# Optimization experiments

Hardware: AMD Instinct MI355X
Metric: run time of the kernel (lower is better)

## Reference

```python
import jax, jax.numpy as jnp
import numpy as np

NBINS = (128, 64, 32)
N_REGIONS = 5000
N_REGIONS_OI = 500
N_POINTS = 262144
SUM_H = sum(NBINS)            # 224
SUM_W = sum(n - 1 for n in NBINS)  # 221


def _spline_level(x, uw_region, uh_pt, local_ix):
    """One quadratic-spline level.
    x: [N] inputs in [0,1); uw_region: [R, n-1] region unnormalized widths;
    uh_pt: [N, n] per-point unnormalized heights (embedding + delta);
    local_ix: [N] int mapping points -> rows of uw_region.
    """
    # region-level widths / bin locations (calculate_widths / calculate_bin_locations)
    widths = jax.nn.softmax(uw_region, axis=-1)                # [R, n-1]
    bl = jnp.cumsum(widths, axis=-1)
    bl = bl.at[:, -1].set(1.0)
    bin_locations = jnp.pad(bl, ((0, 0), (1, 0)))              # [R, n]

    # gather per point (index_select(0, local_region_ix))
    widths_pt = widths[local_ix]                               # [N, n-1]
    bin_loc_pt = bin_locations[local_ix]                       # [N, n]

    # calculate_heights: exp then normalize so trapezoid integral == 1
    he = jnp.exp(uh_pt)                                        # [N, n]
    area = jnp.sum(0.5 * (he[:, :-1] + he[:, 1:]) * widths_pt, axis=-1, keepdims=True)
    heights = he / area                                        # [N, n]

    # calculate_bin_left_cdf
    cdf = jnp.cumsum(0.5 * (heights[:, :-1] + heights[:, 1:]) * widths_pt, axis=-1)
    cdf = cdf.at[:, -1].set(1.0)
    bin_left_cdf = jnp.pad(cdf, ((0, 0), (1, 0)))              # [N, n]

    # searchsorted(bin_locations, x, side='left') - 1, clamped to valid bins
    n = bin_loc_pt.shape[-1]
    bin_idx = jnp.clip(jnp.sum(bin_loc_pt < x[:, None], axis=-1) - 1, 0, n - 2)  # [N]

    take = lambda a, i: jnp.take_along_axis(a, i[:, None], axis=-1)[:, 0]
    in_loc = take(bin_loc_pt, bin_idx)
    in_w = take(widths_pt, bin_idx)
    in_cdf = take(bin_left_cdf, bin_idx)
    h_l = take(heights, bin_idx)
    h_r = take(heights, bin_idx + 1)

    alpha = (x - in_loc) / in_w
    a = 0.5 * (h_r - h_l) * in_w
    b = h_l * in_w
    out = a * alpha * alpha + b * alpha + in_cdf
    logabsdet = jnp.log(alpha * (h_r - h_l) + h_l)
    return out, logabsdet


def setup_inputs() -> dict:
    key = jax.random.key(0)
    k1, k2, k3, k4, k5, k6 = jax.random.split(key, 6)
    x = jax.random.uniform(k1, (N_POINTS,), dtype=jnp.float32)
    regions_oi = jax.random.randint(k2, (N_REGIONS_OI,), 0, N_REGIONS, dtype=jnp.int32)
    local_region_ix = jax.random.randint(k3, (N_POINTS,), 0, N_REGIONS_OI, dtype=jnp.int32)
    delta = jax.random.normal(k4, (N_POINTS, SUM_H), dtype=jnp.float32)
    # learned sparse embedding tables (init to random for a nontrivial baseline)
    heights_emb = 0.1 * jax.random.normal(k5, (N_REGIONS, SUM_H), dtype=jnp.float32)
    widths_emb = 0.1 * jax.random.normal(k6, (N_REGIONS, SUM_W), dtype=jnp.float32)
    return {"x": x, "regions_oi": regions_oi, "local_region_ix": local_region_ix,
            "delta": delta, "heights_emb": heights_emb, "widths_emb": widths_emb}


def reference(x, regions_oi, local_region_ix, delta, heights_emb, widths_emb):
    uh_all = heights_emb[regions_oi]   # [R, 224]
    uw_all = widths_emb[regions_oi]    # [R, 221]
    out = x
    logdet = jnp.zeros_like(x)
    oh = 0
    ow = 0
    for n in NBINS:
        uw = uw_all[:, ow:ow + (n - 1)]                               # [R, n-1]
        uh_pt = uh_all[local_region_ix][:, oh:oh + n] + delta[:, oh:oh + n]  # [N, n]
        out, ld = _spline_level(out, uw, uh_pt, local_region_ix)
        logdet = logdet + ld
        oh += n
        ow += n - 1
    return out, logdet
```

## Files before the change

### kernel.cpp

```cpp
#include <hip/hip_runtime.h>

#define NPOINTS 262144
#define SUMH 224
#define SUMW 221
#define NREG 500

__device__ __forceinline__ float rlane(float v, int l) {
  return __int_as_float(__builtin_amdgcn_readlane(__float_as_int(v), l));
}
template<int CTRL>
__device__ __forceinline__ float dpp0(float x) {
  return __int_as_float(__builtin_amdgcn_update_dpp(0, __float_as_int(x), CTRL, 0xF, 0xF, true));
}
template<int CTRL, int RM>
__device__ __forceinline__ float dpp_rm(float x) {
  return __int_as_float(__builtin_amdgcn_update_dpp(0, __float_as_int(x), CTRL, RM, 0xF, false));
}
template<int CTRL>
__device__ __forceinline__ float dpp_max_(float x) {
  return fmaxf(x, __int_as_float(__builtin_amdgcn_update_dpp(__float_as_int(x), __float_as_int(x), CTRL, 0xF, 0xF, false)));
}
__device__ __forceinline__ float wave_sum(float x) {
  x += dpp0<0x111>(x); x += dpp0<0x112>(x); x += dpp0<0x114>(x); x += dpp0<0x118>(x);
  x += dpp_rm<0x142, 0xA>(x); x += dpp_rm<0x143, 0xC>(x);
  return rlane(x, 63);
}
__device__ __forceinline__ float wave_max(float x) {
  x = dpp_max_<0x111>(x); x = dpp_max_<0x112>(x); x = dpp_max_<0x114>(x);
  x = dpp_max_<0x118>(x); x = dpp_max_<0x142>(x); x = dpp_max_<0x143>(x);
  return rlane(x, 63);
}
__device__ __forceinline__ float wave_scan_incl(float x) {
  x += dpp0<0x111>(x); x += dpp0<0x112>(x); x += dpp0<0x114>(x); x += dpp0<0x118>(x);
  x += dpp_rm<0x142, 0xA>(x);
  x += dpp_rm<0x143, 0xC>(x);
  return x;
}
__device__ __forceinline__ float grp32_sum(float x) {
  x += dpp0<0xB1>(x);
  x += dpp0<0x4E>(x);
  x += dpp0<0x141>(x);
  x += dpp0<0x140>(x);
  x += __int_as_float(__builtin_amdgcn_ds_swizzle(__float_as_int(x), 0x401F));
  return x;
}
__device__ __forceinline__ float bperm(int byteidx, float v) {
  return __int_as_float(__builtin_amdgcn_ds_bpermute(byteidx, __float_as_int(v)));
}

template<int M, int SRC, int DST, int NB>
__device__ __forceinline__ void region_level(const float* __restrict__ wrow,
    float* __restrict__ BL, float* __restrict__ HW, float* __restrict__ HS,
    int lane, float* lds)
{
  float v0 = (lane < M) ? wrow[SRC + lane] : -1e30f;
  float v1 = -1e30f;
  if constexpr (NB == 128) { if (lane + 64 < M) v1 = wrow[SRC + lane + 64]; }
  float m = wave_max(fmaxf(v0, v1));
  float e0 = __expf(v0 - m);
  float e1 = (NB == 128) ? __expf(v1 - m) : 0.0f;
  float sm = wave_sum(e0 + e1);
  float inv = 1.0f / sm;
  if (lane < NB) lds[lane] = e0;
  if constexpr (NB == 128) lds[lane + 64] = e1;
  __syncthreads();
  if (lane < NB) {
    HW[DST + lane] = 0.5f * e0 * inv;
    float prev = (lane == 0) ? 0.0f : lds[lane - 1];
    HS[DST + lane] = 0.5f * (e0 + prev) * inv;
  }
  if constexpr (NB == 128) {
    HW[DST + lane + 64] = 0.5f * e1 * inv;
    HS[DST + lane + 64] = 0.5f * (e1 + lds[lane + 63]) * inv;
  }
  float incl0 = wave_scan_incl(e0);
  if (lane == 0) BL[DST] = 0.0f;
  if (lane < M) BL[DST + 1 + lane] = (lane == M - 1) ? 1.0f : incl0 * inv;
  if constexpr (NB == 128) {
    float incl1 = wave_scan_incl(e1) + rlane(incl0, 63);
    int k = 64 + lane;
    if (k < M) BL[DST + 1 + k] = (k == M - 1) ? 1.0f : incl1 * inv;
  }
  __syncthreads();
}

__global__ void __launch_bounds__(64) region_kernel(
    const int* __restrict__ roi, const float* __restrict__ wemb,
    float* __restrict__ wsBL, float* __restrict__ wsHW, float* __restrict__ wsHS)
{
  __shared__ float lds[128];
  int rix = blockIdx.x;
  int lane = threadIdx.x;
  int greg = roi[rix];
  const float* wrow = wemb + (size_t)greg * SUMW;
  float* BL = wsBL + (size_t)rix * SUMH;
  float* HW = wsHW + (size_t)rix * SUMH;
  float* HS = wsHS + (size_t)rix * SUMH;
  region_level<127,   0,   0, 128>(wrow, BL, HW, HS, lane, lds);
  region_level< 63, 127, 128,  64>(wrow, BL, HW, HS, lane, lds);
  region_level< 31, 190, 192,  32>(wrow, BL, HW, HS, lane, lds);
}


struct PtState {
  float4 a0, b0, e0, f0, g0;
  float2 a1, b1, e1, f1, g1;
  float  a2, b2, e2, f2, g2;
  float  xv;
  int    pid;
};

__device__ __forceinline__ void load_pt(PtState& P, int pid, int s,
    const float* __restrict__ x, const int* __restrict__ lix,
    const int* __restrict__ roi, const float* __restrict__ delta,
    const float* __restrict__ hemb, const float* __restrict__ wsBL,
    const float* __restrict__ wsHW, const float* __restrict__ wsHS)
{
  P.pid = pid;
  P.xv = x[pid];
  int r = lix[pid];
  int greg = roi[r];
  const float* U  = hemb + (size_t)greg * SUMH;
  const float* D  = delta + (size_t)pid * SUMH;
  const float* BL = wsBL + (size_t)r * SUMH;
  const float* HW = wsHW + (size_t)r * SUMH;
  const float* HS = wsHS + (size_t)r * SUMH;
  int c0 = s * 4;
  P.a0 = *(const float4*)(U + c0);  P.b0 = *(const float4*)(D + c0);
  P.e0 = *(const float4*)(BL + c0); P.f0 = *(const float4*)(HW + c0);
  P.g0 = *(const float4*)(HS + c0);
  int c1 = 128 + s * 2;
  P.a1 = *(const float2*)(U + c1);  P.b1 = *(const float2*)(D + c1);
  P.e1 = *(const float2*)(BL + c1); P.f1 = *(const float2*)(HW + c1);
  P.g1 = *(const float2*)(HS + c1);
  int c2 = 192 + s;
  P.a2 = U[c2]; P.b2 = D[c2]; P.e2 = BL[c2]; P.f2 = HW[c2]; P.g2 = HS[c2];
}

template<int C>
__device__ __forceinline__ void apply32(float& xv, float& logdet, int s, int nb_idx,
    const float (&u)[C], const float (&d)[C], const float (&bl)[C],
    const float (&hw)[C], const float (&hs)[C])
{
  float he[C], t[C], f[C];
#pragma unroll
  for (int i = 0; i < C; ++i) { he[i] = __expf(u[i] + d[i]); t[i] = he[i] * hs[i]; }
#pragma unroll
  for (int i = 0; i < C; ++i) f[i] = (bl[i] < xv) ? 1.0f : 0.0f;
  if (s == 0)  f[0]     = 1.0f;
  if (s == 31) f[C - 1] = 0.0f;
  float fN  = bperm(nb_idx, f[0]);
  float heN = bperm(nb_idx, he[0]);
  float area = 0.0f, hl = 0.0f, hr = 0.0f, loc = 0.0f, hwm = 0.0f, pt = 0.0f;
#pragma unroll
  for (int i = 0; i < C; ++i) {
    float fnext  = (i < C - 1) ? f[i + 1]  : fN;
    float henext = (i < C - 1) ? he[i + 1] : heN;
    float mi = f[i] * (1.0f - fnext);
    area += t[i];
    hl  += he[i] * mi;
    hr  += henext * mi;
    loc += bl[i] * mi;
    hwm += hw[i] * mi;
    pt  += t[i] * f[i];
  }
  area = grp32_sum(area);
  hl  = grp32_sum(hl);
  hr  = grp32_sum(hr);
  loc = grp32_sum(loc);
  hwm = grp32_sum(hwm);
  pt  = grp32_sum(pt);
  float larea = __log2f(area);
  float invarea = __builtin_amdgcn_rcpf(area);
  float part = pt - hl * hwm;
  float inw = 2.0f * hwm;
  float alpha = (xv - loc) * __builtin_amdgcn_rcpf(inw);
  float dh = hr - hl;
  xv = ((0.5f * dh * alpha + hl) * alpha * inw + part) * invarea;
  logdet += (__log2f(alpha * dh + hl) - larea) * 0.69314718055994531f;
}

__device__ __forceinline__ void compute_pt(const PtState& P, int s, int nb_idx,
                                           float* __restrict__ out)
{
  float xv = P.xv;
  float logdet = 0.0f;
  {
    float u[4]  = {P.a0.x, P.a0.y, P.a0.z, P.a0.w};
    float d[4]  = {P.b0.x, P.b0.y, P.b0.z, P.b0.w};
    float bl[4] = {P.e0.x, P.e0.y, P.e0.z, P.e0.w};
    float hw[4] = {P.f0.x, P.f0.y, P.f0.z, P.f0.w};
    float hs[4] = {P.g0.x, P.g0.y, P.g0.z, P.g0.w};
    apply32<4>(xv, logdet, s, nb_idx, u, d, bl, hw, hs);
  }
  {
    float u[2]  = {P.a1.x, P.a1.y};
    float d[2]  = {P.b1.x, P.b1.y};
    float bl[2] = {P.e1.x, P.e1.y};
    float hw[2] = {P.f1.x, P.f1.y};
    float hs[2] = {P.g1.x, P.g1.y};
    apply32<2>(xv, logdet, s, nb_idx, u, d, bl, hw, hs);
  }
  {
    float u[1]  = {P.a2};
    float d[1]  = {P.b2};
    float bl[1] = {P.e2};
    float hw[1] = {P.f2};
    float hs[1] = {P.g2};
    apply32<1>(xv, logdet, s, nb_idx, u, d, bl, hw, hs);
  }
  if (s == 0) {
    out[P.pid] = xv;
    out[NPOINTS + P.pid] = logdet;
  }
}

__global__ void __launch_bounds__(256, 4) spline_kernel(
    const float* __restrict__ x, const int* __restrict__ roi,
    const int* __restrict__ lix, const float* __restrict__ delta,
    const float* __restrict__ hemb,
    const float* __restrict__ wsBL, const float* __restrict__ wsHW,
    const float* __restrict__ wsHS, float* __restrict__ out)
{
  int tid  = (int)(blockIdx.x * blockDim.x + threadIdx.x);
  int wid  = tid >> 6;
  int lane = (int)(threadIdx.x & 63);
  int grp  = lane >> 5;
  int s    = lane & 31;
  int base = wid * 4;
  int nb_idx = ((lane + 1) & 63) << 2;

  PtState A, B;
  load_pt(A, base + grp,     s, x, lix, roi, delta, hemb, wsBL, wsHW, wsHS);
  load_pt(B, base + 2 + grp, s, x, lix, roi, delta, hemb, wsBL, wsHW, wsHS);

  compute_pt(A, s, nb_idx, out);
  compute_pt(B, s, nb_idx, out);
}


extern "C" void kernel_launch(void* const* d_in, const int* in_sizes, int n_in,
                              void* d_out, int out_size, void* d_ws, size_t ws_size,
                              hipStream_t stream) {
  const float* x     = (const float*)d_in[0];
  const int*   roi   = (const int*)  d_in[1];
  const int*   lix   = (const int*)  d_in[2];
  const float* delta = (const float*)d_in[3];
  const float* hemb  = (const float*)d_in[4];
  const float* wemb  = (const float*)d_in[5];

  float* wsBL = (float*)d_ws;
  float* wsHW = wsBL + (size_t)NREG * SUMH;
  float* wsHS = wsHW + (size_t)NREG * SUMH;

  region_kernel<<<NREG, 64, 0, stream>>>(roi, wemb, wsBL, wsHW, wsHS);
  spline_kernel<<<NPOINTS / 16, 256, 0, stream>>>(x, roi, lix, delta, hemb,
                                                  wsBL, wsHW, wsHS, (float*)d_out);
}
```

Before: 346.1 us.

## Derive widths from bin locations and replace group reductions with ballot-select permutes

The region kernel now writes only bin locations. The spline kernel reconstructs bin widths and trapezoid terms from neighbouring bin locations, so the two precomputed arrays per region and their per-point loads go away. The four per-bin selection reductions are replaced by a ballot that finds the lane owning the target bin, followed by ds_bpermute reads of its values. The cost is an extra neighbour permute and slightly different rounding from computing widths as differences of cumulative sums.

```diff
diff --git a/kernel.cpp b/kernel.cpp
--- a/kernel.cpp
+++ b/kernel.cpp
@@ -50,8 +50,7 @@
 
 template<int M, int SRC, int DST, int NB>
 __device__ __forceinline__ void region_level(const float* __restrict__ wrow,
-    float* __restrict__ BL, float* __restrict__ HW, float* __restrict__ HS,
-    int lane, float* lds)
+    float* __restrict__ BL, int lane)
 {
   float v0 = (lane < M) ? wrow[SRC + lane] : -1e30f;
   float v1 = -1e30f;
@@ -61,18 +60,6 @@
   float e1 = (NB == 128) ? __expf(v1 - m) : 0.0f;
   float sm = wave_sum(e0 + e1);
   float inv = 1.0f / sm;
-  if (lane < NB) lds[lane] = e0;
-  if constexpr (NB == 128) lds[lane + 64] = e1;
-  __syncthreads();
-  if (lane < NB) {
-    HW[DST + lane] = 0.5f * e0 * inv;
-    float prev = (lane == 0) ? 0.0f : lds[lane - 1];
-    HS[DST + lane] = 0.5f * (e0 + prev) * inv;
-  }
-  if constexpr (NB == 128) {
-    HW[DST + lane + 64] = 0.5f * e1 * inv;
-    HS[DST + lane + 64] = 0.5f * (e1 + lds[lane + 63]) * inv;
-  }
   float incl0 = wave_scan_incl(e0);
   if (lane == 0) BL[DST] = 0.0f;
   if (lane < M) BL[DST + 1 + lane] = (lane == M - 1) ? 1.0f : incl0 * inv;
@@ -81,31 +68,27 @@
     int k = 64 + lane;
     if (k < M) BL[DST + 1 + k] = (k == M - 1) ? 1.0f : incl1 * inv;
   }
-  __syncthreads();
 }
 
 __global__ void __launch_bounds__(64) region_kernel(
     const int* __restrict__ roi, const float* __restrict__ wemb,
-    float* __restrict__ wsBL, float* __restrict__ wsHW, float* __restrict__ wsHS)
-{
-  __shared__ float lds[128];
+    float* __restrict__ wsBL)
+{
   int rix = blockIdx.x;
   int lane = threadIdx.x;
   int greg = roi[rix];
   const float* wrow = wemb + (size_t)greg * SUMW;
   float* BL = wsBL + (size_t)rix * SUMH;
-  float* HW = wsHW + (size_t)rix * SUMH;
-  float* HS = wsHS + (size_t)rix * SUMH;
-  region_level<127,   0,   0, 128>(wrow, BL, HW, HS, lane, lds);
-  region_level< 63, 127, 128,  64>(wrow, BL, HW, HS, lane, lds);
-  region_level< 31, 190, 192,  32>(wrow, BL, HW, HS, lane, lds);
+  region_level<127,   0,   0, 128>(wrow, BL, lane);
+  region_level< 63, 127, 128,  64>(wrow, BL, lane);
+  region_level< 31, 190, 192,  32>(wrow, BL, lane);
 }
 
 
 struct PtState {
-  float4 a0, b0, e0, f0, g0;
-  float2 a1, b1, e1, f1, g1;
-  float  a2, b2, e2, f2, g2;
+  float4 a0, b0, e0;
+  float2 a1, b1, e1;
+  float  a2, b2, e2;
   float  xv;
   int    pid;
 };
@@ -113,8 +96,7 @@
 __device__ __forceinline__ void load_pt(PtState& P, int pid, int s,
     const float* __restrict__ x, const int* __restrict__ lix,
     const int* __restrict__ roi, const float* __restrict__ delta,
-    const float* __restrict__ hemb, const float* __restrict__ wsBL,
-    const float* __restrict__ wsHW, const float* __restrict__ wsHS)
+    const float* __restrict__ hemb, const float* __restrict__ wsBL)
 {
   P.pid = pid;
   P.xv = x[pid];
@@ -123,64 +105,68 @@
   const float* U  = hemb + (size_t)greg * SUMH;
   const float* D  = delta + (size_t)pid * SUMH;
   const float* BL = wsBL + (size_t)r * SUMH;
-  const float* HW = wsHW + (size_t)r * SUMH;
-  const float* HS = wsHS + (size_t)r * SUMH;
   int c0 = s * 4;
   P.a0 = *(const float4*)(U + c0);  P.b0 = *(const float4*)(D + c0);
-  P.e0 = *(const float4*)(BL + c0); P.f0 = *(const float4*)(HW + c0);
-  P.g0 = *(const float4*)(HS + c0);
+  P.e0 = *(const float4*)(BL + c0);
   int c1 = 128 + s * 2;
   P.a1 = *(const float2*)(U + c1);  P.b1 = *(const float2*)(D + c1);
-  P.e1 = *(const float2*)(BL + c1); P.f1 = *(const float2*)(HW + c1);
-  P.g1 = *(const float2*)(HS + c1);
+  P.e1 = *(const float2*)(BL + c1);
   int c2 = 192 + s;
-  P.a2 = U[c2]; P.b2 = D[c2]; P.e2 = BL[c2]; P.f2 = HW[c2]; P.g2 = HS[c2];
+  P.a2 = U[c2]; P.b2 = D[c2]; P.e2 = BL[c2];
 }
 
 template<int C>
-__device__ __forceinline__ void apply32(float& xv, float& logdet, int s, int nb_idx,
-    const float (&u)[C], const float (&d)[C], const float (&bl)[C],
-    const float (&hw)[C], const float (&hs)[C])
-{
-  float he[C], t[C], f[C];
+__device__ __forceinline__ void apply32(float& xv, float& logdet, int s, int gbase, int nb_idx,
+    const float (&u)[C], const float (&d)[C], const float (&bl)[C])
+{
+  float he[C], f[C];
 #pragma unroll
-  for (int i = 0; i < C; ++i) { he[i] = __expf(u[i] + d[i]); t[i] = he[i] * hs[i]; }
+  for (int i = 0; i < C; ++i) he[i] = __expf(u[i] + d[i]);
 #pragma unroll
   for (int i = 0; i < C; ++i) f[i] = (bl[i] < xv) ? 1.0f : 0.0f;
   if (s == 0)  f[0]     = 1.0f;
   if (s == 31) f[C - 1] = 0.0f;
   float fN  = bperm(nb_idx, f[0]);
   float heN = bperm(nb_idx, he[0]);
-  float area = 0.0f, hl = 0.0f, hr = 0.0f, loc = 0.0f, hwm = 0.0f, pt = 0.0f;
+  float blN = bperm(nb_idx, bl[0]);
+  float area = 0.0f, pt = 0.0f;
+  float hl = 0.0f, hr = 0.0f, loc = 0.0f, inw = 0.0f;
+  bool own = false;
 #pragma unroll
   for (int i = 0; i < C; ++i) {
     float fnext  = (i < C - 1) ? f[i + 1]  : fN;
     float henext = (i < C - 1) ? he[i + 1] : heN;
+    float blnext = (i < C - 1) ? bl[i + 1] : blN;
+    float w = blnext - bl[i];
+    if (i == C - 1) w = (s == 31) ? 0.0f : w;
+    float tb = 0.5f * (he[i] + henext) * w;
+    area += tb;
+    pt   += tb * fnext;
     float mi = f[i] * (1.0f - fnext);
-    area += t[i];
-    hl  += he[i] * mi;
+    own = own | (mi != 0.0f);
+    hl  += he[i]  * mi;
     hr  += henext * mi;
-    loc += bl[i] * mi;
-    hwm += hw[i] * mi;
-    pt  += t[i] * f[i];
+    loc += bl[i]  * mi;
+    inw += w      * mi;
   }
   area = grp32_sum(area);
-  hl  = grp32_sum(hl);
-  hr  = grp32_sum(hr);
-  loc = grp32_sum(loc);
-  hwm = grp32_sum(hwm);
-  pt  = grp32_sum(pt);
+  pt   = grp32_sum(pt);
+  unsigned long long m64 = __ballot(own);
+  unsigned gm = gbase ? (unsigned)(m64 >> 32) : (unsigned)m64;
+  int ob = ((__builtin_ctz(gm) + gbase) << 2);
+  hl  = bperm(ob, hl);
+  hr  = bperm(ob, hr);
+  loc = bperm(ob, loc);
+  inw = bperm(ob, inw);
   float larea = __log2f(area);
   float invarea = __builtin_amdgcn_rcpf(area);
-  float part = pt - hl * hwm;
-  float inw = 2.0f * hwm;
   float alpha = (xv - loc) * __builtin_amdgcn_rcpf(inw);
   float dh = hr - hl;
-  xv = ((0.5f * dh * alpha + hl) * alpha * inw + part) * invarea;
+  xv = ((0.5f * dh * alpha + hl) * alpha * inw + pt) * invarea;
   logdet += (__log2f(alpha * dh + hl) - larea) * 0.69314718055994531f;
 }
 
-__device__ __forceinline__ void compute_pt(const PtState& P, int s, int nb_idx,
+__device__ __forceinline__ void compute_pt(const PtState& P, int s, int gbase, int nb_idx,
                                            float* __restrict__ out)
 {
   float xv = P.xv;
@@ -189,25 +175,19 @@
     float u[4]  = {P.a0.x, P.a0.y, P.a0.z, P.a0.w};
     float d[4]  = {P.b0.x, P.b0.y, P.b0.z, P.b0.w};
     float bl[4] = {P.e0.x, P.e0.y, P.e0.z, P.e0.w};
-    float hw[4] = {P.f0.x, P.f0.y, P.f0.z, P.f0.w};
-    float hs[4] = {P.g0.x, P.g0.y, P.g0.z, P.g0.w};
-    apply32<4>(xv, logdet, s, nb_idx, u, d, bl, hw, hs);
+    apply32<4>(xv, logdet, s, gbase, nb_idx, u, d, bl);
   }
   {
     float u[2]  = {P.a1.x, P.a1.y};
     float d[2]  = {P.b1.x, P.b1.y};
     float bl[2] = {P.e1.x, P.e1.y};
-    float hw[2] = {P.f1.x, P.f1.y};
-    float hs[2] = {P.g1.x, P.g1.y};
-    apply32<2>(xv, logdet, s, nb_idx, u, d, bl, hw, hs);
+    apply32<2>(xv, logdet, s, gbase, nb_idx, u, d, bl);
   }
   {
     float u[1]  = {P.a2};
     float d[1]  = {P.b2};
     float bl[1] = {P.e2};
-    float hw[1] = {P.f2};
-    float hs[1] = {P.g2};
-    apply32<1>(xv, logdet, s, nb_idx, u, d, bl, hw, hs);
+    apply32<1>(xv, logdet, s, gbase, nb_idx, u, d, bl);
   }
   if (s == 0) {
     out[P.pid] = xv;
@@ -218,24 +198,24 @@
 __global__ void __launch_bounds__(256, 4) spline_kernel(
     const float* __restrict__ x, const int* __restrict__ roi,
     const int* __restrict__ lix, const float* __restrict__ delta,
-    const float* __restrict__ hemb,
-    const float* __restrict__ wsBL, const float* __restrict__ wsHW,
-    const float* __restrict__ wsHS, float* __restrict__ out)
+    const float* __restrict__ hemb, const float* __restrict__ wsBL,
+    float* __restrict__ out)
 {
   int tid  = (int)(blockIdx.x * blockDim.x + threadIdx.x);
   int wid  = tid >> 6;
   int lane = (int)(threadIdx.x & 63);
   int grp  = lane >> 5;
   int s    = lane & 31;
+  int gbase = lane & 32;
   int base = wid * 4;
   int nb_idx = ((lane + 1) & 63) << 2;
 
   PtState A, B;
-  load_pt(A, base + grp,     s, x, lix, roi, delta, hemb, wsBL, wsHW, wsHS);
-  load_pt(B, base + 2 + grp, s, x, lix, roi, delta, hemb, wsBL, wsHW, wsHS);
-
-  compute_pt(A, s, nb_idx, out);
-  compute_pt(B, s, nb_idx, out);
+  load_pt(A, base + grp,     s, x, lix, roi, delta, hemb, wsBL);
+  load_pt(B, base + 2 + grp, s, x, lix, roi, delta, hemb, wsBL);
+
+  compute_pt(A, s, gbase, nb_idx, out);
+  compute_pt(B, s, gbase, nb_idx, out);
 }
 
 
@@ -250,10 +230,8 @@
   const float* wemb  = (const float*)d_in[5];
 
   float* wsBL = (float*)d_ws;
-  float* wsHW = wsBL + (size_t)NREG * SUMH;
-  float* wsHS = wsHW + (size_t)NREG * SUMH;
-
-  region_kernel<<<NREG, 64, 0, stream>>>(roi, wemb, wsBL, wsHW, wsHS);
+
+  region_kernel<<<NREG, 64, 0, stream>>>(roi, wemb, wsBL);
   spline_kernel<<<NPOINTS / 16, 256, 0, stream>>>(x, roi, lix, delta, hemb,
-                                                  wsBL, wsHW, wsHS, (float*)d_out);
-}
+                                                  wsBL, (float*)d_out);
+}
```

New measurement: 338.2 us. 1.02x faster.
